# Performance work log

Measured on AMD Instinct MI355X. Metric: run time of the kernel, lower is better.

Reference implementation:

```python
import jax, jax.numpy as jnp
import numpy as np

N_USERS = 100000
N_ITEMS = 50000
N_EDGES = 2000000
D = 64


def setup_inputs() -> dict:
    key = jax.random.key(0)
    ks = jax.random.split(key, 8)
    return {
        "user_feat": jax.random.normal(ks[0], (N_USERS, D), dtype=jnp.float32),
        "item_feat": jax.random.normal(ks[1], (N_ITEMS, D), dtype=jnp.float32),
        "norm_ui": jax.random.uniform(ks[2], (N_EDGES, 1), dtype=jnp.float32),
        "norm_iu": jax.random.uniform(ks[3], (N_EDGES, 1), dtype=jnp.float32),
        "ui_src": jax.random.randint(ks[4], (N_EDGES,), 0, N_USERS, dtype=jnp.int32),
        "ui_dst": jax.random.randint(ks[5], (N_EDGES,), 0, N_ITEMS, dtype=jnp.int32),
        "iu_src": jax.random.randint(ks[6], (N_EDGES,), 0, N_ITEMS, dtype=jnp.int32),
        "iu_dst": jax.random.randint(ks[7], (N_EDGES,), 0, N_USERS, dtype=jnp.int32),
    }


def reference(user_feat, item_feat, norm_ui, norm_iu, ui_src, ui_dst, iu_src, iu_dst):
    # relation (user, ui, item): gather user feats, scale by edge norm, scatter-sum to items
    msg_ui = norm_ui * user_feat[ui_src]                       # [E, D]
    h_item = jax.ops.segment_sum(msg_ui, ui_dst, num_segments=N_ITEMS)
    # relation (item, iu, user): gather item feats, scale, scatter-sum to users
    msg_iu = norm_iu * item_feat[iu_src]                       # [E, D]
    h_user = jax.ops.segment_sum(msg_iu, iu_dst, num_segments=N_USERS)
    return h_user, h_item
```

## Files before the change

### kernel.cpp

```cpp
#include <hip/hip_runtime.h>

#define D 64
#define N_USERS 100000
#define N_ITEMS 50000
#define RW 64
#define B_UI ((N_ITEMS + RW - 1) / RW)
#define B_IU ((N_USERS + RW - 1) / RW)
#define B_TOT (B_UI + B_IU)
#define CHUNK 8192
#define SCT_THREADS 1024
#define P2_THREADS 512
#define TILE 4096

static inline size_t align16(size_t x) { return (x + 15) & ~(size_t)15; }

__device__ inline unsigned int bf16rne(float f) {
    unsigned int b = __float_as_uint(f);
    return (b + 0x7fffu + ((b >> 16) & 1u)) >> 16;
}
__device__ inline float bf16lo(unsigned int u) { return __uint_as_float(u << 16); }
__device__ inline float bf16hi(unsigned int u) { return __uint_as_float(u & 0xffff0000u); }

__global__ void convert_feats_kernel(const float* __restrict__ user_feat,
                                     const float* __restrict__ item_feat,
                                     unsigned int* __restrict__ user16,
                                     unsigned int* __restrict__ item16) {
    const long long USER_ELEMS = (long long)N_USERS * D;
    const long long TOTAL = USER_ELEMS + (long long)N_ITEMS * D;
    long long i4 = ((long long)blockIdx.x * blockDim.x + threadIdx.x) * 4;
    const long long stride = (long long)gridDim.x * blockDim.x * 4;
    for (; i4 < TOTAL; i4 += stride) {
        const float4 v = (i4 < USER_ELEMS)
            ? *(const float4*)(user_feat + i4)
            : *(const float4*)(item_feat + (i4 - USER_ELEMS));
        uint2 p;
        p.x = bf16rne(v.x) | (bf16rne(v.y) << 16);
        p.y = bf16rne(v.z) | (bf16rne(v.w) << 16);
        unsigned int* dst = (i4 < USER_ELEMS) ? (user16 + (i4 >> 1))
                                              : (item16 + ((i4 - USER_ELEMS) >> 1));
        *(uint2*)dst = p;
    }
}

__global__ void count_totals_kernel(const int* __restrict__ ui_dst,
                                    const int* __restrict__ iu_dst,
                                    int* __restrict__ totals,
                                    int n_ui, long long n_total) {
    __shared__ int hist[B_TOT];
    for (int b = threadIdx.x; b < B_TOT; b += blockDim.x) hist[b] = 0;
    __syncthreads();
    long long i = (long long)blockIdx.x * blockDim.x + threadIdx.x;
    const long long stride = (long long)gridDim.x * blockDim.x;
    for (; i < n_total; i += stride) {
        const int b = (i < n_ui) ? (ui_dst[i] >> 6)
                                 : B_UI + (iu_dst[i - n_ui] >> 6);
        atomicAdd(&hist[b], 1);
    }
    __syncthreads();
    for (int b = threadIdx.x; b < B_TOT; b += blockDim.x) {
        const int c = hist[b];
        if (c) atomicAdd(&totals[b], c);
    }
}

__global__ void scan_totals_kernel(const int* __restrict__ totals,
                                   int* __restrict__ base,
                                   int* __restrict__ gcur) {
    __shared__ int lds[1024];
    const int t = threadIdx.x;
    int v[3];
    int s = 0;
#pragma unroll
    for (int k = 0; k < 3; k++) {
        const int i = t * 3 + k;
        v[k] = (i < B_TOT) ? totals[i] : 0;
        s += v[k];
    }
    lds[t] = s;
    __syncthreads();
    for (int off = 1; off < 1024; off <<= 1) {
        int x = (t >= off) ? lds[t - off] : 0;
        __syncthreads();
        lds[t] += x;
        __syncthreads();
    }
    int run = lds[t] - s;
#pragma unroll
    for (int k = 0; k < 3; k++) {
        const int i = t * 3 + k;
        if (i < B_TOT) { base[i] = run; gcur[i] = run; }
        else if (i == B_TOT) { base[i] = run; }
        run += v[k];
    }
}

__global__ __launch_bounds__(SCT_THREADS) void p1_scatter_kernel(
                                  const int* __restrict__ ui_src,
                                  const int* __restrict__ iu_src,
                                  const int* __restrict__ ui_dst,
                                  const int* __restrict__ iu_dst,
                                  const float* __restrict__ norm_ui,
                                  const float* __restrict__ norm_iu,
                                  int* __restrict__ gcur,
                                  long long* __restrict__ part,
                                  int n_ui, int n_iu, int NB_ui) {
    __shared__ int lcnt[B_IU];
    __shared__ int lcur[B_IU];
    const int blk = blockIdx.x;
    const bool is_ui = blk < NB_ui;
    const int* src = is_ui ? ui_src : iu_src;
    const int* dst = is_ui ? ui_dst : iu_dst;
    const float* nrm = is_ui ? norm_ui : norm_iu;
    const int n = is_ui ? n_ui : n_iu;
    const int sideB = is_ui ? B_UI : B_IU;
    const int boff = is_ui ? 0 : B_UI;
    const int e0 = (is_ui ? blk : blk - NB_ui) * CHUNK;

    for (int b = threadIdx.x; b < sideB; b += blockDim.x) lcnt[b] = 0;
    __syncthreads();
    for (int k = 0; k < CHUNK; k += blockDim.x) {
        const int t = e0 + k + threadIdx.x;
        if (t < n) atomicAdd(&lcnt[dst[t] >> 6], 1);
    }
    __syncthreads();
    for (int b = threadIdx.x; b < sideB; b += blockDim.x) {
        const int c = lcnt[b];
        lcur[b] = c ? atomicAdd(&gcur[boff + b], c) : 0;
    }
    __syncthreads();
    for (int k = 0; k < CHUNK; k += blockDim.x) {
        const int t = e0 + k + threadIdx.x;
        if (t < n) {
            const int d = dst[t];
            const int pos = atomicAdd(&lcur[d >> 6], 1);
            const unsigned int lo = (unsigned int)(src[t] | ((d & 63) << 26));
            const unsigned int hi = (unsigned int)__float_as_int(nrm[t]);
            part[pos] = (long long)(((unsigned long long)hi << 32) | lo);
        }
    }
}

__global__ __launch_bounds__(P2_THREADS, 6) void p2_gather_kernel(
        const uint4* __restrict__ user16, const uint4* __restrict__ item16,
        const long long* __restrict__ part, const int* __restrict__ base,
        float* __restrict__ h_user, float* __restrict__ h_item) {
    __shared__ int2 sorted[TILE];
    __shared__ float acc[RW * D];
    __shared__ int cnt[RW], offs[RW], cursor[RW], cnt2[RW];
    const int b = blockIdx.x;
    const int tid = threadIdx.x;
    const int lane = tid & 63;
    const int wave = tid >> 6;

    const int E0 = base[b];
    const int E1 = base[b + 1];

    const bool item_side = b < B_UI;
    const uint4* __restrict__ feat = item_side ? user16 : item16;
    const int baseRow = (item_side ? b : b - B_UI) * RW;

    for (int i = tid; i < RW * D; i += P2_THREADS) acc[i] = 0.f;

    for (int bas = E0; bas < E1; bas += TILE) {
        const int tileN = min(TILE, E1 - bas);
        if (tid < RW) cnt[tid] = 0;
        __syncthreads();
        int2 v[TILE / P2_THREADS];
#pragma unroll
        for (int k = 0; k < TILE / P2_THREADS; k++) {
            const int t = tid + k * P2_THREADS;
            if (t < tileN) {
                const long long raw = __builtin_nontemporal_load(&part[bas + t]);
                v[k].x = (int)(unsigned int)(raw & 0xffffffffll);
                v[k].y = (int)(unsigned int)((unsigned long long)raw >> 32);
                atomicAdd(&cnt[((unsigned)v[k].x) >> 26], 1);
            }
        }
        __syncthreads();
        if (tid < RW) {
            const int c = cnt[tid];
            int incl = c;
            for (int dd = 1; dd < RW; dd <<= 1) {
                const int u = __shfl_up(incl, dd, 64);
                if (lane >= dd) incl += u;
            }
            offs[tid] = incl - c;
            cursor[tid] = incl - c;
            cnt2[tid] = c;
        }
        __syncthreads();
#pragma unroll
        for (int k = 0; k < TILE / P2_THREADS; k++) {
            const int t = tid + k * P2_THREADS;
            if (t < tileN) {
                const int r6 = ((unsigned)v[k].x) >> 26;
                const int pos = atomicAdd(&cursor[r6], 1);
                sorted[pos] = v[k];
            }
        }
        __syncthreads();
        for (int r = wave; r < RW; r += 8) {
            const int s = offs[r], c = cnt2[r];
            if (c == 0) continue;
            const int sub = lane & 7;
            const int g = lane >> 3;
            float a0 = 0, a1 = 0, a2 = 0, a3 = 0, a4 = 0, a5 = 0, a6 = 0, a7 = 0;
            for (int j = g; j < c; j += 32) {
                const int2 e0 = sorted[s + j];
                const int2 e1 = (j + 8  < c) ? sorted[s + j + 8]  : make_int2(0, 0);
                const int2 e2 = (j + 16 < c) ? sorted[s + j + 16] : make_int2(0, 0);
                const int2 e3 = (j + 24 < c) ? sorted[s + j + 24] : make_int2(0, 0);
                const uint4 f0 = feat[(e0.x & 0x03FFFFFF) * 8 + sub];
                const uint4 f1 = feat[(e1.x & 0x03FFFFFF) * 8 + sub];
                const uint4 f2 = feat[(e2.x & 0x03FFFFFF) * 8 + sub];
                const uint4 f3 = feat[(e3.x & 0x03FFFFFF) * 8 + sub];
                const float n0 = __int_as_float(e0.y);
                const float n1 = __int_as_float(e1.y);
                const float n2 = __int_as_float(e2.y);
                const float n3 = __int_as_float(e3.y);
                a0 = fmaf(n0, bf16lo(f0.x), a0);
                a1 = fmaf(n0, bf16hi(f0.x), a1);
                a2 = fmaf(n0, bf16lo(f0.y), a2);
                a3 = fmaf(n0, bf16hi(f0.y), a3);
                a4 = fmaf(n0, bf16lo(f0.z), a4);
                a5 = fmaf(n0, bf16hi(f0.z), a5);
                a6 = fmaf(n0, bf16lo(f0.w), a6);
                a7 = fmaf(n0, bf16hi(f0.w), a7);
                a0 = fmaf(n1, bf16lo(f1.x), a0);
                a1 = fmaf(n1, bf16hi(f1.x), a1);
                a2 = fmaf(n1, bf16lo(f1.y), a2);
                a3 = fmaf(n1, bf16hi(f1.y), a3);
                a4 = fmaf(n1, bf16lo(f1.z), a4);
                a5 = fmaf(n1, bf16hi(f1.z), a5);
                a6 = fmaf(n1, bf16lo(f1.w), a6);
                a7 = fmaf(n1, bf16hi(f1.w), a7);
                a0 = fmaf(n2, bf16lo(f2.x), a0);
                a1 = fmaf(n2, bf16hi(f2.x), a1);
                a2 = fmaf(n2, bf16lo(f2.y), a2);
                a3 = fmaf(n2, bf16hi(f2.y), a3);
                a4 = fmaf(n2, bf16lo(f2.z), a4);
                a5 = fmaf(n2, bf16hi(f2.z), a5);
                a6 = fmaf(n2, bf16lo(f2.w), a6);
                a7 = fmaf(n2, bf16hi(f2.w), a7);
                a0 = fmaf(n3, bf16lo(f3.x), a0);
                a1 = fmaf(n3, bf16hi(f3.x), a1);
                a2 = fmaf(n3, bf16lo(f3.y), a2);
                a3 = fmaf(n3, bf16hi(f3.y), a3);
                a4 = fmaf(n3, bf16lo(f3.z), a4);
                a5 = fmaf(n3, bf16hi(f3.z), a5);
                a6 = fmaf(n3, bf16lo(f3.w), a6);
                a7 = fmaf(n3, bf16hi(f3.w), a7);
            }
            for (int m = 8; m <= 32; m <<= 1) {
                a0 += __shfl_xor(a0, m, 64);
                a1 += __shfl_xor(a1, m, 64);
                a2 += __shfl_xor(a2, m, 64);
                a3 += __shfl_xor(a3, m, 64);
                a4 += __shfl_xor(a4, m, 64);
                a5 += __shfl_xor(a5, m, 64);
                a6 += __shfl_xor(a6, m, 64);
                a7 += __shfl_xor(a7, m, 64);
            }
            if (lane < 8) {
                float4* ap = (float4*)&acc[r * D + lane * 8];
                float4 q0 = ap[0], q1 = ap[1];
                q0.x += a0; q0.y += a1; q0.z += a2; q0.w += a3;
                q1.x += a4; q1.y += a5; q1.z += a6; q1.w += a7;
                ap[0] = q0; ap[1] = q1;
            }
        }
    }
    __syncthreads();
    float* __restrict__ outp = item_side ? h_item : h_user;
    const int limit = item_side ? N_ITEMS : N_USERS;
#pragma unroll
    for (int it = 0; it < 1024 / P2_THREADS; it++) {
        const int i4 = tid + it * P2_THREADS;
        const int r = (i4 * 4) >> 6;
        const int row = baseRow + r;
        if (row < limit) {
            *(float4*)&outp[(long long)row * D + ((i4 * 4) & 63)] = *(float4*)&acc[i4 * 4];
        }
    }
}

__global__ void scatter_rel_kernel(const float* __restrict__ feat,
                                   const float* __restrict__ norm,
                                   const int* __restrict__ src,
                                   const int* __restrict__ dst,
                                   float* __restrict__ out, int n_edges) {
    const int lane = threadIdx.x & 63;
    const int wib = threadIdx.x >> 6;
    const int wpb = blockDim.x >> 6;
    long long e = (long long)blockIdx.x * wpb + wib;
    const long long stride = (long long)gridDim.x * wpb;
    for (; e < n_edges; e += stride) {
        atomicAdd(&out[(long long)dst[e] * D + lane],
                  norm[e] * feat[(long long)src[e] * D + lane]);
    }
}

extern "C" void kernel_launch(void* const* d_in, const int* in_sizes, int n_in,
                              void* d_out, int out_size, void* d_ws, size_t ws_size,
                              hipStream_t stream) {
    const float* user_feat = (const float*)d_in[0];
    const float* item_feat = (const float*)d_in[1];
    const float* norm_ui   = (const float*)d_in[2];
    const float* norm_iu   = (const float*)d_in[3];
    const int*   ui_src    = (const int*)d_in[4];
    const int*   ui_dst    = (const int*)d_in[5];
    const int*   iu_src    = (const int*)d_in[6];
    const int*   iu_dst    = (const int*)d_in[7];

    const int n_ui = in_sizes[4];
    const int n_iu = in_sizes[6];
    const int n_total = n_ui + n_iu;

    float* h_user = (float*)d_out;
    float* h_item = (float*)d_out + (long long)N_USERS * D;

    const int block = 256;
    const int NB_ui = (n_ui + CHUNK - 1) / CHUNK;
    const int NB_iu = (n_iu + CHUNK - 1) / CHUNK;
    const int NB = NB_ui + NB_iu;

    char* ws = (char*)d_ws;
    size_t off = 0;
    int* totals = (int*)(ws + off);  off += align16((size_t)B_TOT * 4);
    int* base   = (int*)(ws + off);  off += align16((size_t)(B_TOT + 1) * 4);
    int* gcur   = (int*)(ws + off);  off += align16((size_t)B_TOT * 4);
    long long* part = (long long*)(ws + off); off += align16((size_t)n_total * 8);
    unsigned int* user16 = (unsigned int*)(ws + off); off += align16((size_t)N_USERS * D * 2);
    unsigned int* item16 = (unsigned int*)(ws + off); off += align16((size_t)N_ITEMS * D * 2);
    const size_t needed = off;

    if (ws_size < needed) {
        hipMemsetAsync(d_out, 0, (size_t)out_size * sizeof(float), stream);
        const int wpb = block / 64;
        scatter_rel_kernel<<<(n_ui + wpb - 1) / wpb, block, 0, stream>>>(
            user_feat, norm_ui, ui_src, ui_dst, h_item, n_ui);
        scatter_rel_kernel<<<(n_iu + wpb - 1) / wpb, block, 0, stream>>>(
            item_feat, norm_iu, iu_src, iu_dst, h_user, n_iu);
        return;
    }

    hipMemsetAsync(totals, 0, (size_t)B_TOT * 4, stream);

    const long long cv_threads = ((long long)(N_USERS + N_ITEMS) * D) / 4;
    convert_feats_kernel<<<(int)((cv_threads + block - 1) / block), block, 0, stream>>>(
        user_feat, item_feat, user16, item16);

    count_totals_kernel<<<512, block, 0, stream>>>(ui_dst, iu_dst, totals,
                                                   n_ui, (long long)n_total);

    scan_totals_kernel<<<1, 1024, 0, stream>>>(totals, base, gcur);

    p1_scatter_kernel<<<NB, SCT_THREADS, 0, stream>>>(ui_src, iu_src, ui_dst, iu_dst,
                                                      norm_ui, norm_iu, gcur, part,
                                                      n_ui, n_iu, NB_ui);

    p2_gather_kernel<<<B_TOT, P2_THREADS, 0, stream>>>(
        (const uint4*)user16, (const uint4*)item16, part, base,
        h_user, h_item);
}
```

Measured before the change: 343.9 us.

## Fuse feature conversion with histogram count, and fold scan into scatter kernel

The bf16 feature conversion and the destination-bucket histogram now run in one kernel, launched with a fixed grid of 512 blocks. The single-block prefix-scan kernel is removed: every scatter block redundantly scans the totals itself and adds a global atomic offset counter, zeroed by the memset, to get its write positions. This cuts two kernel launches and their serialization gaps. In exchange, each block repeats a 1024-wide scan and holds larger shared histograms covering all buckets.

Result: faster. 336.8 us (-2.1%).

```diff
diff --git a/kernel.cpp b/kernel.cpp
--- a/kernel.cpp
+++ b/kernel.cpp
@@ -21,40 +21,41 @@
 __device__ inline float bf16lo(unsigned int u) { return __uint_as_float(u << 16); }
 __device__ inline float bf16hi(unsigned int u) { return __uint_as_float(u & 0xffff0000u); }
 
-__global__ void convert_feats_kernel(const float* __restrict__ user_feat,
-                                     const float* __restrict__ item_feat,
-                                     unsigned int* __restrict__ user16,
-                                     unsigned int* __restrict__ item16) {
+__global__ __launch_bounds__(256) void convert_count_kernel(
+        const float* __restrict__ user_feat, const float* __restrict__ item_feat,
+        unsigned int* __restrict__ user16, unsigned int* __restrict__ item16,
+        const int* __restrict__ ui_dst, const int* __restrict__ iu_dst,
+        int* __restrict__ totals, int n_ui, long long n_total) {
+    __shared__ int hist[B_TOT];
+    for (int b = threadIdx.x; b < B_TOT; b += blockDim.x) hist[b] = 0;
+    __syncthreads();
+
     const long long USER_ELEMS = (long long)N_USERS * D;
     const long long TOTAL = USER_ELEMS + (long long)N_ITEMS * D;
-    long long i4 = ((long long)blockIdx.x * blockDim.x + threadIdx.x) * 4;
-    const long long stride = (long long)gridDim.x * blockDim.x * 4;
-    for (; i4 < TOTAL; i4 += stride) {
-        const float4 v = (i4 < USER_ELEMS)
-            ? *(const float4*)(user_feat + i4)
-            : *(const float4*)(item_feat + (i4 - USER_ELEMS));
-        uint2 p;
-        p.x = bf16rne(v.x) | (bf16rne(v.y) << 16);
-        p.y = bf16rne(v.z) | (bf16rne(v.w) << 16);
-        unsigned int* dst = (i4 < USER_ELEMS) ? (user16 + (i4 >> 1))
-                                              : (item16 + ((i4 - USER_ELEMS) >> 1));
-        *(uint2*)dst = p;
-    }
-}
-
-__global__ void count_totals_kernel(const int* __restrict__ ui_dst,
-                                    const int* __restrict__ iu_dst,
-                                    int* __restrict__ totals,
-                                    int n_ui, long long n_total) {
-    __shared__ int hist[B_TOT];
-    for (int b = threadIdx.x; b < B_TOT; b += blockDim.x) hist[b] = 0;
-    __syncthreads();
-    long long i = (long long)blockIdx.x * blockDim.x + threadIdx.x;
-    const long long stride = (long long)gridDim.x * blockDim.x;
-    for (; i < n_total; i += stride) {
-        const int b = (i < n_ui) ? (ui_dst[i] >> 6)
-                                 : B_UI + (iu_dst[i - n_ui] >> 6);
-        atomicAdd(&hist[b], 1);
+    {
+        long long i4 = ((long long)blockIdx.x * blockDim.x + threadIdx.x) * 4;
+        const long long stride = (long long)gridDim.x * blockDim.x * 4;
+        for (; i4 < TOTAL; i4 += stride) {
+            const float4 v = (i4 < USER_ELEMS)
+                ? *(const float4*)(user_feat + i4)
+                : *(const float4*)(item_feat + (i4 - USER_ELEMS));
+            uint2 p;
+            p.x = bf16rne(v.x) | (bf16rne(v.y) << 16);
+            p.y = bf16rne(v.z) | (bf16rne(v.w) << 16);
+            unsigned int* dst = (i4 < USER_ELEMS) ? (user16 + (i4 >> 1))
+                                                  : (item16 + ((i4 - USER_ELEMS) >> 1));
+            *(uint2*)dst = p;
+        }
+    }
+
+    {
+        long long i = (long long)blockIdx.x * blockDim.x + threadIdx.x;
+        const long long stride = (long long)gridDim.x * blockDim.x;
+        for (; i < n_total; i += stride) {
+            const int b = (i < n_ui) ? (ui_dst[i] >> 6)
+                                     : B_UI + (iu_dst[i - n_ui] >> 6);
+            atomicAdd(&hist[b], 1);
+        }
     }
     __syncthreads();
     for (int b = threadIdx.x; b < B_TOT; b += blockDim.x) {
@@ -63,79 +64,82 @@
     }
 }
 
-__global__ void scan_totals_kernel(const int* __restrict__ totals,
-                                   int* __restrict__ base,
-                                   int* __restrict__ gcur) {
+__global__ __launch_bounds__(SCT_THREADS) void p1_scan_scatter_kernel(
+        const int* __restrict__ ui_src, const int* __restrict__ iu_src,
+        const int* __restrict__ ui_dst, const int* __restrict__ iu_dst,
+        const float* __restrict__ norm_ui, const float* __restrict__ norm_iu,
+        const int* __restrict__ totals,
+        int* __restrict__ base,
+        int* __restrict__ gcur0,
+        long long* __restrict__ part,
+        int n_ui, int n_iu, int NB_ui, int NCH) {
+    __shared__ int lcnt[B_TOT];
+    __shared__ int lcur[B_TOT];
     __shared__ int lds[1024];
-    const int t = threadIdx.x;
-    int v[3];
-    int s = 0;
-#pragma unroll
-    for (int k = 0; k < 3; k++) {
-        const int i = t * 3 + k;
-        v[k] = (i < B_TOT) ? totals[i] : 0;
-        s += v[k];
-    }
-    lds[t] = s;
-    __syncthreads();
-    for (int off = 1; off < 1024; off <<= 1) {
-        int x = (t >= off) ? lds[t - off] : 0;
-        __syncthreads();
-        lds[t] += x;
-        __syncthreads();
-    }
-    int run = lds[t] - s;
-#pragma unroll
-    for (int k = 0; k < 3; k++) {
-        const int i = t * 3 + k;
-        if (i < B_TOT) { base[i] = run; gcur[i] = run; }
-        else if (i == B_TOT) { base[i] = run; }
-        run += v[k];
-    }
-}
-
-__global__ __launch_bounds__(SCT_THREADS) void p1_scatter_kernel(
-                                  const int* __restrict__ ui_src,
-                                  const int* __restrict__ iu_src,
-                                  const int* __restrict__ ui_dst,
-                                  const int* __restrict__ iu_dst,
-                                  const float* __restrict__ norm_ui,
-                                  const float* __restrict__ norm_iu,
-                                  int* __restrict__ gcur,
-                                  long long* __restrict__ part,
-                                  int n_ui, int n_iu, int NB_ui) {
-    __shared__ int lcnt[B_IU];
-    __shared__ int lcur[B_IU];
-    const int blk = blockIdx.x;
-    const bool is_ui = blk < NB_ui;
-    const int* src = is_ui ? ui_src : iu_src;
-    const int* dst = is_ui ? ui_dst : iu_dst;
-    const float* nrm = is_ui ? norm_ui : norm_iu;
-    const int n = is_ui ? n_ui : n_iu;
-    const int sideB = is_ui ? B_UI : B_IU;
-    const int boff = is_ui ? 0 : B_UI;
-    const int e0 = (is_ui ? blk : blk - NB_ui) * CHUNK;
-
-    for (int b = threadIdx.x; b < sideB; b += blockDim.x) lcnt[b] = 0;
-    __syncthreads();
-    for (int k = 0; k < CHUNK; k += blockDim.x) {
-        const int t = e0 + k + threadIdx.x;
-        if (t < n) atomicAdd(&lcnt[dst[t] >> 6], 1);
-    }
-    __syncthreads();
-    for (int b = threadIdx.x; b < sideB; b += blockDim.x) {
+    const int tid = threadIdx.x;
+
+    {
+        int v0, v1, v2;
+        const int i0 = tid * 3;
+        v0 = (i0 + 0 < B_TOT) ? totals[i0 + 0] : 0;
+        v1 = (i0 + 1 < B_TOT) ? totals[i0 + 1] : 0;
+        v2 = (i0 + 2 < B_TOT) ? totals[i0 + 2] : 0;
+        const int s = v0 + v1 + v2;
+        lds[tid] = s;
+        __syncthreads();
+        for (int off = 1; off < 1024; off <<= 1) {
+            int x = (tid >= off) ? lds[tid - off] : 0;
+            __syncthreads();
+            lds[tid] += x;
+            __syncthreads();
+        }
+        int run = lds[tid] - s;
+        const bool pub = (blockIdx.x == 0);
+        if (i0 + 0 < B_TOT) { lcur[i0 + 0] = run; if (pub) base[i0 + 0] = run; } else if (i0 + 0 == B_TOT && pub) base[B_TOT] = run;
+        run += v0;
+        if (i0 + 1 < B_TOT) { lcur[i0 + 1] = run; if (pub) base[i0 + 1] = run; } else if (i0 + 1 == B_TOT && pub) base[B_TOT] = run;
+        run += v1;
+        if (i0 + 2 < B_TOT) { lcur[i0 + 2] = run; if (pub) base[i0 + 2] = run; } else if (i0 + 2 == B_TOT && pub) base[B_TOT] = run;
+    }
+    for (int b = tid; b < B_TOT; b += SCT_THREADS) lcnt[b] = 0;
+    __syncthreads();
+
+    for (int c = blockIdx.x; c < NCH; c += gridDim.x) {
+        const bool is_ui = c < NB_ui;
+        const int* dst = is_ui ? ui_dst : iu_dst;
+        const int n = is_ui ? n_ui : n_iu;
+        const int boff = is_ui ? 0 : B_UI;
+        const int e0 = (is_ui ? c : c - NB_ui) * CHUNK;
+        for (int k = 0; k < CHUNK; k += SCT_THREADS) {
+            const int t = e0 + k + tid;
+            if (t < n) atomicAdd(&lcnt[boff + (dst[t] >> 6)], 1);
+        }
+    }
+    __syncthreads();
+
+    for (int b = tid; b < B_TOT; b += SCT_THREADS) {
         const int c = lcnt[b];
-        lcur[b] = c ? atomicAdd(&gcur[boff + b], c) : 0;
-    }
-    __syncthreads();
-    for (int k = 0; k < CHUNK; k += blockDim.x) {
-        const int t = e0 + k + threadIdx.x;
-        if (t < n) {
-            const int d = dst[t];
-            const int pos = atomicAdd(&lcur[d >> 6], 1);
-            const unsigned int lo = (unsigned int)(src[t] | ((d & 63) << 26));
-            const unsigned int hi = (unsigned int)__float_as_int(nrm[t]);
-            part[pos] = (long long)(((unsigned long long)hi << 32) | lo);
+        if (c) lcur[b] += atomicAdd(&gcur0[b], c);
+    }
+    __syncthreads();
+
+    for (int c = blockIdx.x; c < NCH; c += gridDim.x) {
+        const bool is_ui = c < NB_ui;
+        const int* src = is_ui ? ui_src : iu_src;
+        const int* dst = is_ui ? ui_dst : iu_dst;
+        const float* nrm = is_ui ? norm_ui : norm_iu;
+        const int n = is_ui ? n_ui : n_iu;
+        const int boff = is_ui ? 0 : B_UI;
+        const int e0 = (is_ui ? c : c - NB_ui) * CHUNK;
+        for (int k = 0; k < CHUNK; k += SCT_THREADS) {
+            const int t = e0 + k + tid;
+            if (t < n) {
+                const int d = dst[t];
+                const int pos = atomicAdd(&lcur[boff + (d >> 6)], 1);
+                const unsigned int lo = (unsigned int)(src[t] | ((d & 63) << 26));
+                const unsigned int hi = (unsigned int)__float_as_int(nrm[t]);
+                part[pos] = (long long)(((unsigned long long)hi << 32) | lo);
+            }
         }
     }
 }
@@ -322,13 +326,13 @@
     const int block = 256;
     const int NB_ui = (n_ui + CHUNK - 1) / CHUNK;
     const int NB_iu = (n_iu + CHUNK - 1) / CHUNK;
-    const int NB = NB_ui + NB_iu;
+    const int NCH = NB_ui + NB_iu;
 
     char* ws = (char*)d_ws;
     size_t off = 0;
     int* totals = (int*)(ws + off);  off += align16((size_t)B_TOT * 4);
+    int* gcur0  = (int*)(ws + off);  off += align16((size_t)B_TOT * 4);
     int* base   = (int*)(ws + off);  off += align16((size_t)(B_TOT + 1) * 4);
-    int* gcur   = (int*)(ws + off);  off += align16((size_t)B_TOT * 4);
     long long* part = (long long*)(ws + off); off += align16((size_t)n_total * 8);
     unsigned int* user16 = (unsigned int*)(ws + off); off += align16((size_t)N_USERS * D * 2);
     unsigned int* item16 = (unsigned int*)(ws + off); off += align16((size_t)N_ITEMS * D * 2);
@@ -344,20 +348,15 @@
         return;
     }
 
-    hipMemsetAsync(totals, 0, (size_t)B_TOT * 4, stream);
-
-    const long long cv_threads = ((long long)(N_USERS + N_ITEMS) * D) / 4;
-    convert_feats_kernel<<<(int)((cv_threads + block - 1) / block), block, 0, stream>>>(
-        user_feat, item_feat, user16, item16);
-
-    count_totals_kernel<<<512, block, 0, stream>>>(ui_dst, iu_dst, totals,
-                                                   n_ui, (long long)n_total);
-
-    scan_totals_kernel<<<1, 1024, 0, stream>>>(totals, base, gcur);
-
-    p1_scatter_kernel<<<NB, SCT_THREADS, 0, stream>>>(ui_src, iu_src, ui_dst, iu_dst,
-                                                      norm_ui, norm_iu, gcur, part,
-                                                      n_ui, n_iu, NB_ui);
+    hipMemsetAsync(totals, 0, ((size_t)align16((size_t)B_TOT * 4) + (size_t)B_TOT * 4), stream);
+
+    convert_count_kernel<<<512, block, 0, stream>>>(
+        user_feat, item_feat, user16, item16, ui_dst, iu_dst,
+        totals, n_ui, (long long)n_total);
+
+    p1_scan_scatter_kernel<<<NCH, SCT_THREADS, 0, stream>>>(
+        ui_src, iu_src, ui_dst, iu_dst, norm_ui, norm_iu,
+        totals, base, gcur0, part, n_ui, n_iu, NB_ui, NCH);
 
     p2_gather_kernel<<<B_TOT, P2_THREADS, 0, stream>>>(
         (const uint4*)user16, (const uint4*)item16, part, base,
```
